# Kernel optimization log

Measured on AMD Instinct MI355X. Metric: run time of the kernel, lower is better.

Reference implementation:

```python
import jax, jax.numpy as jnp
from jax import lax
import numpy as np

B = 32768
H = 7
W = 7
EMB = 64
NUM_ACTIONS = 7
HIDDEN = 128
CNN_OUT = 64 * 3 * 3  # 576, from 7x7 input through the conv/pool stack


def setup_inputs() -> dict:
    key = jax.random.key(0)
    ks = jax.random.split(key, 20)
    frame = jax.random.randint(ks[0], (2, B, H, W, 3), 0, 11, dtype=jnp.int32)
    carried_col = jax.random.randint(ks[1], (2, B, 1), 0, 6, dtype=jnp.int32)
    carried_obj = jax.random.randint(ks[2], (2, B, 1), 0, 11, dtype=jnp.int32)

    def w(k, shape):
        return (jax.random.normal(k, shape, jnp.float32) * 0.05)

    return {
        "frame": frame,
        "carried_col": carried_col,
        "carried_obj": carried_obj,
        "conv1_w": w(ks[3], (16, 3, 2, 2)),  "conv1_b": jnp.zeros((16,), jnp.float32),
        "conv2_w": w(ks[4], (32, 16, 2, 2)), "conv2_b": jnp.zeros((32,), jnp.float32),
        "conv3_w": w(ks[5], (64, 32, 2, 2)), "conv3_b": jnp.zeros((64,), jnp.float32),
        "proj_w": w(ks[6], (EMB, CNN_OUT + 2)), "proj_b": jnp.zeros((EMB,), jnp.float32),
        "h1_w": w(ks[7], (HIDDEN, EMB * 2 + 4)), "h1_b": jnp.zeros((HIDDEN,), jnp.float32),
        "ln_g": jnp.ones((HIDDEN,), jnp.float32), "ln_b": jnp.zeros((HIDDEN,), jnp.float32),
        "h2_w": w(ks[8], (HIDDEN, HIDDEN)), "h2_b": jnp.zeros((HIDDEN,), jnp.float32),
        "h3_w": w(ks[9], (NUM_ACTIONS, HIDDEN)), "h3_b": jnp.zeros((NUM_ACTIONS,), jnp.float32),
    }


def _conv(x, wgt, b):
    # Conv2d(kernel=2, padding=1), NCHW
    y = lax.conv_general_dilated(x, wgt, (1, 1), [(1, 1), (1, 1)],
                                 dimension_numbers=("NCHW", "OIHW", "NCHW"))
    return y + b[None, :, None, None]


def _maxpool2(x):
    # MaxPool2d(2): window 2, stride 2, floor (VALID)
    return lax.reduce_window(x, -jnp.inf, lax.max, (1, 1, 2, 2), (1, 1, 2, 2), "VALID")


def _encode(fr, cc, co, p):
    x = fr.transpose(0, 3, 1, 2).astype(jnp.float32)  # [B,3,H,W]
    x = _maxpool2(jax.nn.relu(_conv(x, p["conv1_w"], p["conv1_b"])))  # [B,16,4,4]
    x = _maxpool2(jax.nn.relu(_conv(x, p["conv2_w"], p["conv2_b"])))  # [B,32,2,2]
    x = jax.nn.relu(_conv(x, p["conv3_w"], p["conv3_b"]))             # [B,64,3,3]
    feats = x.reshape(x.shape[0], -1)                                  # [B,576]
    carried = jnp.concatenate([cc, co], axis=-1).astype(jnp.float32)   # [B,2]
    comb = jnp.concatenate([feats, carried], axis=1)                   # [B,578]
    return jax.nn.relu(comb @ p["proj_w"].T + p["proj_b"])            # [B,64]


def _dir_pos(fr):
    # vectorized first-match of frame[...,0]==10 in row-major order
    b = fr.shape[0]
    mask = (fr[..., 0] == 10).reshape(b, -1)             # [B, H*W]
    has = jnp.any(mask, axis=-1)                         # [B]
    idx = jnp.argmax(mask, axis=-1)                      # first True (row-major)
    y = idx // W
    x = idx % W
    ch2 = fr[..., 2].reshape(b, -1)
    d_raw = jnp.take_along_axis(ch2, idx[:, None], axis=1)[:, 0] % 4
    d = jnp.where(has, d_raw, 0)                         # [B] int
    pos = jnp.stack([y.astype(jnp.float32) / (H - 1),
                     x.astype(jnp.float32) / (W - 1)], axis=-1)
    pos = jnp.where(has[:, None], pos, jnp.float32(0.5))  # [B,2]
    return d, pos


def _forward(frame, carried_col, carried_obj, p):
    curr_f, next_f = frame[0], frame[1]
    curr_emb = _encode(curr_f, carried_col[0], carried_obj[0], p)
    next_emb = _encode(next_f, carried_col[1], carried_obj[1], p)
    cd, cpos = _dir_pos(curr_f)
    nd, npos = _dir_pos(next_f)
    delta = ((nd - cd + 4) % 4).astype(jnp.float32)
    angle = delta * (2.0 * 3.14159 / 4.0)  # matches source constant
    dir_delta = jnp.stack([jnp.sin(angle), jnp.cos(angle)], axis=-1)  # [B,2]
    pos_delta = npos - cpos                                           # [B,2]
    comb = jnp.concatenate([curr_emb, next_emb, dir_delta, pos_delta], axis=-1)  # [B,132]
    h = comb @ p["h1_w"].T + p["h1_b"]
    mu = h.mean(-1, keepdims=True)
    var = ((h - mu) ** 2).mean(-1, keepdims=True)
    h = (h - mu) * lax.rsqrt(var + 1e-5) * p["ln_g"] + p["ln_b"]
    h = jax.nn.relu(h)  # dropout = identity in eval
    h = jax.nn.relu(h @ p["h2_w"].T + p["h2_b"])
    return h @ p["h3_w"].T + p["h3_b"]  # [B, num_actions]


def reference(frame, carried_col, carried_obj,
              conv1_w, conv1_b, conv2_w, conv2_b, conv3_w, conv3_b,
              proj_w, proj_b, h1_w, h1_b, ln_g, ln_b,
              h2_w, h2_b, h3_w, h3_b):
    p = dict(conv1_w=conv1_w, conv1_b=conv1_b, conv2_w=conv2_w, conv2_b=conv2_b,
             conv3_w=conv3_w, conv3_b=conv3_b, proj_w=proj_w, proj_b=proj_b,
             h1_w=h1_w, h1_b=h1_b, ln_g=ln_g, ln_b=ln_b,
             h2_w=h2_w, h2_b=h2_b, h3_w=h3_w, h3_b=h3_b)
    return _forward(frame, carried_col, carried_obj, p)
```

## Files before the change

### kernel.cpp

```cpp
#include <hip/hip_runtime.h>
#include <hip/hip_bf16.h>

#define BATCH 32768
#define NELEM 65536

typedef unsigned short u16;
typedef unsigned int u32;
typedef __attribute__((ext_vector_type(8))) short bf16x8;
typedef __attribute__((ext_vector_type(4))) float f32x4;

__device__ __forceinline__ float bf2f(u16 u) {
    union { u32 u; float f; } c; c.u = ((u32)u) << 16; return c.f;
}
__device__ __forceinline__ u16 f2bf(float f) {
    union { float f; u32 u; } c; c.f = f;
    u32 x = c.u;
    u32 r = (x + 0x7fffu + ((x >> 16) & 1u)) >> 16;
    return (u16)r;
}

__global__ __launch_bounds__(256) void k0_prep(const float* __restrict__ pw,
        const float* __restrict__ w2, const float* __restrict__ w3,
        const float* __restrict__ h2w, const float* __restrict__ h1w,
        const float* __restrict__ w1,
        u16* __restrict__ pwT, u16* __restrict__ w2r, u16* __restrict__ w3r,
        u16* __restrict__ h2hi, u16* __restrict__ h2lo,
        u16* __restrict__ h1hi, u16* __restrict__ h1lo,
        u16* __restrict__ w1hi, u16* __restrict__ w1lo) {
    int idx = blockIdx.x * 256 + threadIdx.x;
    if (idx < 38912) {
        int j = idx / 608, kk = idx - j * 608;
        float v = 0.f;
        if (kk < 576) {
            int p = kk >> 6, oc = kk & 63;
            v = pw[j * 578 + oc * 9 + p];
        } else if (kk < 578) {
            v = pw[j * 578 + kk];
        }
        pwT[idx] = f2bf(v);
    } else if (idx < 40960) {
        int i = idx - 38912;
        int oc = i >> 6, rem = i & 63, tap = rem >> 4, ic = rem & 15;
        w2r[i] = f2bf(w2[oc * 64 + ic * 4 + tap]);
    } else if (idx < 49152) {
        int i = idx - 40960;
        int oc = i >> 7, rem = i & 127, tap = rem >> 5, ic = rem & 31;
        w3r[i] = f2bf(w3[oc * 128 + ic * 4 + tap]);
    } else if (idx < 65536) {
        int i = idx - 49152;
        float v = h2w[i];
        u16 hi = f2bf(v);
        h2hi[i] = hi;
        h2lo[i] = f2bf(v - bf2f(hi));
    } else if (idx < 86016) {
        int i = idx - 65536;
        int j = i / 160, k = i - j * 160;
        float v = (k < 132) ? h1w[j * 132 + k] : 0.f;
        u16 hi = f2bf(v);
        h1hi[i] = hi;
        h1lo[i] = f2bf(v - bf2f(hi));
    } else if (idx < 86528) {
        int i = idx - 86016;
        int oc = i >> 5, k = i & 31;
        int ky = k >> 4, kx = (k >> 3) & 1, c = k & 7;
        float v = (c < 3) ? w1[oc * 12 + c * 4 + ky * 2 + kx] : 0.f;
        u16 hi = f2bf(v);
        w1hi[i] = hi;
        w1lo[i] = f2bf(v - bf2f(hi));
    }
}

__device__ __forceinline__ void split8(const float* __restrict__ x,
                                       bf16x8& hi, bf16x8& lo) {
    #pragma unroll
    for (int j = 0; j < 8; ++j) {
        u16 h = f2bf(x[j]);
        hi[j] = (short)h;
        lo[j] = (short)f2bf(x[j] - bf2f(h));
    }
}

__global__ __launch_bounds__(256) void kall(const int* __restrict__ frame,
        const u16* __restrict__ w1hi, const u16* __restrict__ w1lo,
        const float* __restrict__ b1,
        const u16* __restrict__ w2r, const float* __restrict__ b2,
        const u16* __restrict__ w3r, const float* __restrict__ b3,
        const int* __restrict__ ccol, const int* __restrict__ cobj,
        const u16* __restrict__ pwT, const float* __restrict__ pb,
        const u16* __restrict__ h1hi, const u16* __restrict__ h1lo,
        const float* __restrict__ h1b,
        const float* __restrict__ lng, const float* __restrict__ lnb,
        const u16* __restrict__ h2hi, const u16* __restrict__ h2lo,
        const float* __restrict__ h2b,
        const float* __restrict__ h3w, const float* __restrict__ h3b,
        float* __restrict__ out) {
    __shared__ u16 lds[24576];
    __shared__ float4 fdirL[32];
    u16* p2L   = lds;
    u16* p1L   = lds + 4096;
    u16* frL   = lds + 12288;
    u16* featL = lds + 4096;
    float* combL = (float*)lds;
    float* hL    = (float*)(lds + 4096);
    int t = threadIdx.x;
    int l = t & 63;
    int wv = t >> 6;
    int col = l & 15;
    int kg = l >> 4;
    int b0 = blockIdx.x * 16;

    #pragma unroll
    for (int i = 0; i < 6; ++i) {
        int o = i * 256 + t;
        if (o < 1312) *(uint4*)(frL + o * 8) = make_uint4(0u, 0u, 0u, 0u);
    }

    {
        bf16x8 c1hi = *(const bf16x8*)(w1hi + col * 32 + kg * 8);
        bf16x8 c1lo = *(const bf16x8*)(w1lo + col * 32 + kg * 8);
        float c1b = b1[col];
        int ky1 = kg >> 1, kx1 = kg & 1;
        bool wr1 = (kg < 2);
        for (int h = 0; h < 2; ++h) {
            __syncthreads();
            const int* fbase = frame + ((size_t)b0 + (size_t)h * BATCH) * 147;
            #pragma unroll
            for (int i = 0; i < 10; ++i) {
                int idx = i * 256 + t;
                if (idx < 2352) {
                    int le = idx / 147, r = idx - le * 147;
                    int cell = r / 3, c = r - cell * 3;
                    int y = cell / 7, x = cell - y * 7;
                    frL[le * 656 + (y + 1) * 72 + (x + 1) * 8 + c] = f2bf((float)fbase[idx]);
                }
            }
            __syncthreads();
            #pragma unroll
            for (int q = 0; q < 4; ++q) {
                int le = wv * 4 + q;
                const u16* eb = frL + le * 656;
                u16* op = p1L + (h * 16 + le) * 256;
                #pragma unroll
                for (int mt = 0; mt < 4; ++mt) {
                    int posA = mt * 16 + col;
                    int oy = posA >> 3, ox = posA & 7;
                    bf16x8 a = *(const bf16x8*)(eb + (oy + ky1) * 72 + (ox + kx1) * 8);
                    f32x4 acc = {0.f, 0.f, 0.f, 0.f};
                    acc = __builtin_amdgcn_mfma_f32_16x16x32_bf16(a, c1hi, acc, 0, 0, 0);
                    acc = __builtin_amdgcn_mfma_f32_16x16x32_bf16(a, c1lo, acc, 0, 0, 0);
                    float x0 = fmaxf(acc[0] + c1b, 0.f);
                    float x1 = fmaxf(acc[1] + c1b, 0.f);
                    float x2 = fmaxf(acc[2] + c1b, 0.f);
                    float x3 = fmaxf(acc[3] + c1b, 0.f);
                    float y0 = fmaxf(x0, x1);
                    float y1 = fmaxf(x2, x3);
                    float m0 = fmaxf(y0, __shfl_xor(y0, 32, 64));
                    float m1 = fmaxf(y1, __shfl_xor(y1, 32, 64));
                    if (wr1) {
                        op[(mt * 4 + kg * 2 + 0) * 16 + col] = f2bf(m0);
                        op[(mt * 4 + kg * 2 + 1) * 16 + col] = f2bf(m1);
                    }
                }
            }
            {
                int le = wv * 4 + kg;
                const u16* eb = frL + le * 656;
                int best = 49;
                #pragma unroll
                for (int q2 = 0; q2 < 4; ++q2) {
                    int cell = col + q2 * 16;
                    if (cell < 49) {
                        int y = cell / 7, x = cell - y * 7;
                        u16 v = eb[(y + 1) * 72 + (x + 1) * 8];
                        if (v == (u16)0x4120 && cell < best) best = cell;
                    }
                }
                best = min(best, __shfl_xor(best, 1, 64));
                best = min(best, __shfl_xor(best, 2, 64));
                best = min(best, __shfl_xor(best, 4, 64));
                best = min(best, __shfl_xor(best, 8, 64));
                if (col == 0) {
                    float dd = 0.f, py = 0.5f, px = 0.5f;
                    if (best < 49) {
                        int y = best / 7, x = best - y * 7;
                        u16 c2 = eb[(y + 1) * 72 + (x + 1) * 8 + 2];
                        dd = (float)(((int)bf2f(c2)) & 3);
                        py = (float)y / 6.0f;
                        px = (float)x / 6.0f;
                    }
                    fdirL[h * 16 + le] = make_float4(dd, py, px, 0.f);
                }
            }
        }
    }
    __syncthreads();

    {
        bf16x8 bfrag[2][2];
        #pragma unroll
        for (int s = 0; s < 2; ++s)
            #pragma unroll
            for (int nt = 0; nt < 2; ++nt)
                bfrag[s][nt] = *(const bf16x8*)(w2r + (nt * 16 + col) * 64 + s * 32 + kg * 8);
        float bias2[2] = { b2[col], b2[16 + col] };
        int oy = col >> 2, ox = col & 3;
        int aoff[2]; bool aok[2];
        #pragma unroll
        for (int s = 0; s < 2; ++s) {
            int tap = 2 * s + (kg >> 1);
            int ky = tap >> 1, kx = tap & 1;
            int iy = oy - 1 + ky, ix = ox - 1 + kx;
            aok[s] = (iy >= 0 && ix >= 0);
            aoff[s] = (iy * 4 + ix) * 16 + (kg & 1) * 8;
        }
        #pragma unroll
        for (int q = 0; q < 8; ++q) {
            int e = wv * 8 + q;
            const u16* pbase = p1L + e * 256;
            bf16x8 a0 = {0,0,0,0,0,0,0,0}, a1 = {0,0,0,0,0,0,0,0};
            if (aok[0]) a0 = *(const bf16x8*)(pbase + aoff[0]);
            if (aok[1]) a1 = *(const bf16x8*)(pbase + aoff[1]);
            f32x4 acc0 = {0.f,0.f,0.f,0.f}, acc1 = {0.f,0.f,0.f,0.f};
            acc0 = __builtin_amdgcn_mfma_f32_16x16x32_bf16(a0, bfrag[0][0], acc0, 0, 0, 0);
            acc1 = __builtin_amdgcn_mfma_f32_16x16x32_bf16(a0, bfrag[0][1], acc1, 0, 0, 0);
            acc0 = __builtin_amdgcn_mfma_f32_16x16x32_bf16(a1, bfrag[1][0], acc0, 0, 0, 0);
            acc1 = __builtin_amdgcn_mfma_f32_16x16x32_bf16(a1, bfrag[1][1], acc1, 0, 0, 0);
            #pragma unroll
            for (int nt = 0; nt < 2; ++nt) {
                f32x4 acc = nt ? acc1 : acc0;
                float b = bias2[nt];
                float m0 = fmaxf(fmaxf(acc[0] + b, 0.f), fmaxf(acc[1] + b, 0.f));
                float m1 = fmaxf(fmaxf(acc[2] + b, 0.f), fmaxf(acc[3] + b, 0.f));
                float p0 = fmaxf(m0, __shfl_xor(m0, 16, 64));
                float p1 = fmaxf(m1, __shfl_xor(m1, 16, 64));
                if ((kg & 1) == 0) {
                    int qq = (kg >> 1) * 2;
                    u16* op = p2L + e * 128 + nt * 16 + col;
                    op[qq * 32]       = f2bf(p0);
                    op[(qq + 1) * 32] = f2bf(p1);
                }
            }
        }
    }
    __syncthreads();

    int colhi = col >> 3, collo = col & 7;
    {
        bf16x8 bfrag[4][4];
        #pragma unroll
        for (int s = 0; s < 4; ++s)
            #pragma unroll
            for (int nt = 0; nt < 4; ++nt)
                bfrag[s][nt] = *(const bf16x8*)(w3r + (nt * 16 + col) * 128 + s * 32 + kg * 8);
        float bias[4];
        #pragma unroll
        for (int nt = 0; nt < 4; ++nt) bias[nt] = b3[nt * 16 + col];

        auto do_tile = [&](int i) {
            int m0 = i * 16;
            int m = m0 + col;
            u32 elem = (u32)(((unsigned long long)(u32)m * 954437177ull) >> 33);
            int p = m - (int)elem * 9;
            int oy = (p * 86) >> 8;
            int ox = p - 3 * oy;
            const u16* pbase = p2L + elem * 128 + kg * 8;
            f32x4 acc[4];
            #pragma unroll
            for (int nt = 0; nt < 4; ++nt) {
                acc[nt][0] = 0.f; acc[nt][1] = 0.f; acc[nt][2] = 0.f; acc[nt][3] = 0.f;
            }
            #pragma unroll
            for (int s = 0; s < 4; ++s) {
                int ky = s >> 1, kx = s & 1;
                int iy = oy - 1 + ky, ix = ox - 1 + kx;
                bf16x8 a = {0,0,0,0,0,0,0,0};
                if (iy >= 0 && iy <= 1 && ix >= 0 && ix <= 1)
                    a = *(const bf16x8*)(pbase + (iy * 2 + ix) * 32);
                #pragma unroll
                for (int nt = 0; nt < 4; ++nt)
                    acc[nt] = __builtin_amdgcn_mfma_f32_16x16x32_bf16(a, bfrag[s][nt], acc[nt], 0, 0, 0);
            }
            #pragma unroll
            for (int r = 0; r < 4; ++r) {
                int mr = m0 + kg * 4 + r;
                u32 er = (u32)(((unsigned long long)(u32)mr * 954437177ull) >> 33);
                int pr = mr - (int)er * 9;
                int e7 = (int)(er & 7u);
                u16* fb = featL + er * 640 + collo;
                #pragma unroll
                for (int nt = 0; nt < 4; ++nt) {
                    int blk = (pr * 8 + nt * 2 + colhi) ^ e7;
                    fb[blk * 8] = f2bf(fmaxf(acc[nt][r] + bias[nt], 0.f));
                }
            }
        };
        #pragma unroll
        for (int u = 0; u < 4; ++u) do_tile(wv + u * 4);
        if (wv < 2) do_tile(16 + wv);
    }
    if (t < 32) {
        int g = b0 + (t >> 4) * BATCH + (t & 15);
        union { u16 s[8]; uint4 q; } b;
        b.s[0] = f2bf((float)ccol[g]);
        b.s[1] = f2bf((float)cobj[g]);
        #pragma unroll
        for (int i = 2; i < 8; ++i) b.s[i] = 0;
        *(uint4*)(featL + t * 640 + (72 ^ (t & 7)) * 8) = b.q;
    }
    __syncthreads();

    {
        int rh = wv & 1, nh = wv >> 1;
        const u16* arowb = featL + (rh * 16 + col) * 640;
        int rx = col & 7;
        const u16* brow = pwT + (nh * 32 + col) * 608 + kg * 8;
        f32x4 acc0 = {0.f,0.f,0.f,0.f}, acc1 = {0.f,0.f,0.f,0.f};
        #pragma unroll
        for (int k0 = 0; k0 < 608; k0 += 32) {
            bf16x8 a;
            if (k0 + kg * 8 < 584) {
                int L = (k0 >> 3) + kg;
                a = *(const bf16x8*)(arowb + (L ^ rx) * 8);
            } else {
                #pragma unroll
                for (int j = 0; j < 8; ++j) a[j] = 0;
            }
            bf16x8 b0f = *(const bf16x8*)(brow + k0);
            bf16x8 b1f = *(const bf16x8*)(brow + 16 * 608 + k0);
            acc0 = __builtin_amdgcn_mfma_f32_16x16x32_bf16(a, b0f, acc0, 0, 0, 0);
            acc1 = __builtin_amdgcn_mfma_f32_16x16x32_bf16(a, b1f, acc1, 0, 0, 0);
        }
        __syncthreads();
        #pragma unroll
        for (int nt = 0; nt < 2; ++nt) {
            int n = nh * 32 + nt * 16 + col;
            float pbv = pb[n];
            f32x4 acc = nt ? acc1 : acc0;
            #pragma unroll
            for (int r = 0; r < 4; ++r) {
                combL[(kg * 4 + r) * 128 + rh * 64 + n] = fmaxf(acc[r] + pbv, 0.f);
            }
        }
    }
    __syncthreads();

    {
        const float* arow = combL + col * 128 + kg * 8;
        f32x4 acc[2];
        acc[0][0]=0.f; acc[0][1]=0.f; acc[0][2]=0.f; acc[0][3]=0.f;
        acc[1][0]=0.f; acc[1][1]=0.f; acc[1][2]=0.f; acc[1][3]=0.f;
        #pragma unroll
        for (int s = 0; s < 5; ++s) {
            float x[8];
            if (s < 4) {
                #pragma unroll
                for (int j = 0; j < 8; ++j) x[j] = arow[s * 32 + j];
            } else {
                #pragma unroll
                for (int j = 0; j < 8; ++j) x[j] = 0.f;
                if (kg == 0) {
                    float4 f0 = fdirL[col];
                    float4 f1 = fdirL[16 + col];
                    int delta = (((int)f1.x) - ((int)f0.x) + 4) & 3;
                    const float ANG = (float)(2.0 * 3.14159 / 4.0);
                    float angle = (float)delta * ANG;
                    x[0] = sinf(angle);
                    x[1] = cosf(angle);
                    x[2] = f1.y - f0.y;
                    x[3] = f1.z - f0.z;
                }
            }
            bf16x8 ahi, alo;
            split8(x, ahi, alo);
            #pragma unroll
            for (int nt = 0; nt < 2; ++nt) {
                int n0 = (wv * 2 + nt) * 16 + col;
                bf16x8 bhiF = *(const bf16x8*)(h1hi + n0 * 160 + s * 32 + kg * 8);
                bf16x8 bloF = *(const bf16x8*)(h1lo + n0 * 160 + s * 32 + kg * 8);
                acc[nt] = __builtin_amdgcn_mfma_f32_16x16x32_bf16(ahi, bhiF, acc[nt], 0, 0, 0);
                acc[nt] = __builtin_amdgcn_mfma_f32_16x16x32_bf16(alo, bhiF, acc[nt], 0, 0, 0);
                acc[nt] = __builtin_amdgcn_mfma_f32_16x16x32_bf16(ahi, bloF, acc[nt], 0, 0, 0);
            }
        }
        #pragma unroll
        for (int nt = 0; nt < 2; ++nt) {
            int n = (wv * 2 + nt) * 16 + col;
            float bv = h1b[n];
            #pragma unroll
            for (int r = 0; r < 4; ++r)
                hL[(kg * 4 + r) * 132 + n] = acc[nt][r] + bv;
        }
    }
    __syncthreads();

    #pragma unroll
    for (int rr = 0; rr < 4; ++rr) {
        float* rp = hL + (wv * 4 + rr) * 132 + l * 2;
        float2 v = *(const float2*)rp;
        float s = v.x + v.y;
        s += __shfl_xor(s, 1, 64);
        s += __shfl_xor(s, 2, 64);
        s += __shfl_xor(s, 4, 64);
        s += __shfl_xor(s, 8, 64);
        s += __shfl_xor(s, 16, 64);
        s += __shfl_xor(s, 32, 64);
        float mu = s * (1.0f / 128.0f);
        float d0 = v.x - mu, d1 = v.y - mu;
        float vs = d0 * d0 + d1 * d1;
        vs += __shfl_xor(vs, 1, 64);
        vs += __shfl_xor(vs, 2, 64);
        vs += __shfl_xor(vs, 4, 64);
        vs += __shfl_xor(vs, 8, 64);
        vs += __shfl_xor(vs, 16, 64);
        vs += __shfl_xor(vs, 32, 64);
        float rs = rsqrtf(vs * (1.0f / 128.0f) + 1e-5f);
        float2 o;
        o.x = fmaxf(d0 * rs * lng[l * 2]     + lnb[l * 2],     0.f);
        o.y = fmaxf(d1 * rs * lng[l * 2 + 1] + lnb[l * 2 + 1], 0.f);
        *(float2*)rp = o;
    }
    __syncthreads();

    {
        const float* arow = hL + col * 132 + kg * 8;
        f32x4 acc[2];
        acc[0][0]=0.f; acc[0][1]=0.f; acc[0][2]=0.f; acc[0][3]=0.f;
        acc[1][0]=0.f; acc[1][1]=0.f; acc[1][2]=0.f; acc[1][3]=0.f;
        #pragma unroll
        for (int s = 0; s < 4; ++s) {
            float x[8];
            #pragma unroll
            for (int j = 0; j < 8; ++j) x[j] = arow[s * 32 + j];
            bf16x8 ahi, alo;
            split8(x, ahi, alo);
            #pragma unroll
            for (int nt = 0; nt < 2; ++nt) {
                int n0 = (wv * 2 + nt) * 16 + col;
                bf16x8 bhiF = *(const bf16x8*)(h2hi + n0 * 128 + s * 32 + kg * 8);
                bf16x8 bloF = *(const bf16x8*)(h2lo + n0 * 128 + s * 32 + kg * 8);
                acc[nt] = __builtin_amdgcn_mfma_f32_16x16x32_bf16(ahi, bhiF, acc[nt], 0, 0, 0);
                acc[nt] = __builtin_amdgcn_mfma_f32_16x16x32_bf16(alo, bhiF, acc[nt], 0, 0, 0);
                acc[nt] = __builtin_amdgcn_mfma_f32_16x16x32_bf16(ahi, bloF, acc[nt], 0, 0, 0);
            }
        }
        __syncthreads();
        #pragma unroll
        for (int nt = 0; nt < 2; ++nt) {
            int n = (wv * 2 + nt) * 16 + col;
            float bv = h2b[n];
            #pragma unroll
            for (int r = 0; r < 4; ++r)
                hL[(kg * 4 + r) * 132 + n] = fmaxf(acc[nt][r] + bv, 0.f);
        }
    }
    __syncthreads();

    if (t < 112) {
        int row = t / 7, j = t - row * 7;
        const float* rp = hL + row * 132;
        float a0 = h3b[j];
        const float* wr0 = h3w + j * 128;
        #pragma unroll 4
        for (int c = 0; c < 32; ++c) {
            float4 v = *(const float4*)(rp + c * 4);
            a0 += v.x * wr0[c * 4 + 0];
            a0 += v.y * wr0[c * 4 + 1];
            a0 += v.z * wr0[c * 4 + 2];
            a0 += v.w * wr0[c * 4 + 3];
        }
        out[(size_t)(b0 + row) * 7 + j] = a0;
    }
}

extern "C" void kernel_launch(void* const* d_in, const int* in_sizes, int n_in,
                              void* d_out, int out_size, void* d_ws, size_t ws_size,
                              hipStream_t stream) {
    const int*   frame = (const int*)d_in[0];
    const int*   ccol  = (const int*)d_in[1];
    const int*   cobj  = (const int*)d_in[2];
    const float* w1    = (const float*)d_in[3];
    const float* b1    = (const float*)d_in[4];
    const float* w2    = (const float*)d_in[5];
    const float* b2    = (const float*)d_in[6];
    const float* w3    = (const float*)d_in[7];
    const float* b3    = (const float*)d_in[8];
    const float* pw    = (const float*)d_in[9];
    const float* pb    = (const float*)d_in[10];
    const float* h1w   = (const float*)d_in[11];
    const float* h1b   = (const float*)d_in[12];
    const float* lng   = (const float*)d_in[13];
    const float* lnb   = (const float*)d_in[14];
    const float* h2w   = (const float*)d_in[15];
    const float* h2b   = (const float*)d_in[16];
    const float* h3w   = (const float*)d_in[17];
    const float* h3b   = (const float*)d_in[18];
    float* out = (float*)d_out;

    char* ws = (char*)d_ws;
    u16*   pwT      = (u16*)(ws + 0);
    u16*   w2r      = (u16*)(ws + 131072);
    u16*   w3r      = (u16*)(ws + 139264);
    u16*   h2hi     = (u16*)(ws + 163840);
    u16*   h2lo     = (u16*)(ws + 196608);
    u16*   h1hi     = (u16*)(ws + 229376);
    u16*   h1lo     = (u16*)(ws + 270336);
    u16*   w1hi     = (u16*)(ws + 311296);
    u16*   w1lo     = (u16*)(ws + 312320);

    k0_prep<<<340, 256, 0, stream>>>(pw, w2, w3, h2w, h1w, w1,
                                     pwT, w2r, w3r, h2hi, h2lo, h1hi, h1lo,
                                     w1hi, w1lo);
    kall<<<2048, 256, 0, stream>>>(frame, w1hi, w1lo, b1, w2r, b2,
                                   w3r, b3, ccol, cobj, pwT, pb,
                                   h1hi, h1lo, h1b, lng, lnb,
                                   h2hi, h2lo, h2b, h3w, h3b, out);
}
```

Baseline: 222.5 us.

## Double block threads, compact frame layout, pre-split bf16 activations in LDS for MLP

Raises the block size from 256 to 512 threads with launch bounds of (512, 6) and shrinks LDS use. The frame layout is compacted to 4 channels per cell, and both frames are loaded in a single pass with vectorized bf16 conversion. The per-wave split of MLP work is redistributed, and the XOR swizzle on the feature buffer is removed in favor of a 584-stride layout. Activations for h1 and h2 are stored in LDS already split into hi/lo bf16, so the per-lane split8 conversion disappears. The trade-offs are possible LDS bank conflicts from the dropped swizzle and tighter register budgets at the higher occupancy target.

```diff
diff --git a/kernel.cpp b/kernel.cpp
--- a/kernel.cpp
+++ b/kernel.cpp
@@ -2,7 +2,6 @@
 #include <hip/hip_bf16.h>
 
 #define BATCH 32768
-#define NELEM 65536
 
 typedef unsigned short u16;
 typedef unsigned int u32;
@@ -17,6 +16,10 @@
     u32 x = c.u;
     u32 r = (x + 0x7fffu + ((x >> 16) & 1u)) >> 16;
     return (u16)r;
+}
+__device__ __forceinline__ u16 i2bf(int v) {
+    union { float f; u32 u; } c; c.f = (float)v;
+    return (u16)(c.u >> 16);
 }
 
 __global__ __launch_bounds__(256) void k0_prep(const float* __restrict__ pw,
@@ -62,25 +65,15 @@
     } else if (idx < 86528) {
         int i = idx - 86016;
         int oc = i >> 5, k = i & 31;
-        int ky = k >> 4, kx = (k >> 3) & 1, c = k & 7;
-        float v = (c < 3) ? w1[oc * 12 + c * 4 + ky * 2 + kx] : 0.f;
+        int ky = k >> 3, kx = (k >> 2) & 1, c = k & 3;
+        float v = (ky < 2 && c < 3) ? w1[oc * 12 + c * 4 + ky * 2 + kx] : 0.f;
         u16 hi = f2bf(v);
         w1hi[i] = hi;
         w1lo[i] = f2bf(v - bf2f(hi));
     }
 }
 
-__device__ __forceinline__ void split8(const float* __restrict__ x,
-                                       bf16x8& hi, bf16x8& lo) {
-    #pragma unroll
-    for (int j = 0; j < 8; ++j) {
-        u16 h = f2bf(x[j]);
-        hi[j] = (short)h;
-        lo[j] = (short)f2bf(x[j] - bf2f(h));
-    }
-}
-
-__global__ __launch_bounds__(256) void kall(const int* __restrict__ frame,
+__global__ __launch_bounds__(512, 6) void kall(const int* __restrict__ frame,
         const u16* __restrict__ w1hi, const u16* __restrict__ w1lo,
         const float* __restrict__ b1,
         const u16* __restrict__ w2r, const float* __restrict__ b2,
@@ -94,102 +87,120 @@
         const float* __restrict__ h2b,
         const float* __restrict__ h3w, const float* __restrict__ h3b,
         float* __restrict__ out) {
-    __shared__ u16 lds[24576];
+    __shared__ u16 lds[22784];
     __shared__ float4 fdirL[32];
-    u16* p2L   = lds;
-    u16* p1L   = lds + 4096;
-    u16* frL   = lds + 12288;
-    u16* featL = lds + 4096;
-    float* combL = (float*)lds;
-    float* hL    = (float*)(lds + 4096);
+    u16* p2L    = lds;
+    u16* p1L    = lds + 4096;
+    u16* frL4   = lds + 12288;
+    u16* featL  = lds + 4096;
+    u16* combHi = lds;
+    u16* combLo = lds + 2560;
+    float* hL   = (float*)(lds + 5120);
+    u16* hLhi   = lds + 9344;
+    u16* hLlo   = lds + 11904;
+
     int t = threadIdx.x;
     int l = t & 63;
     int wv = t >> 6;
     int col = l & 15;
     int kg = l >> 4;
+    int wq = wv & 3, wh = wv >> 2;
     int b0 = blockIdx.x * 16;
 
     #pragma unroll
-    for (int i = 0; i < 6; ++i) {
-        int o = i * 256 + t;
-        if (o < 1312) *(uint4*)(frL + o * 8) = make_uint4(0u, 0u, 0u, 0u);
-    }
+    for (int i = 0; i < 3; ++i) {
+        int o = i * 512 + t;
+        if (o < 1312) *(uint4*)(frL4 + o * 8) = make_uint4(0u, 0u, 0u, 0u);
+    }
+    __syncthreads();
+
+    #pragma unroll
+    for (int i = 0; i < 4; ++i) {
+        int c = i * 512 + t;
+        if (c < 1568) {
+            int le = c / 49, rem = c - le * 49;
+            int y = rem / 7, x = rem - y * 7;
+            const int* fp = frame
+                + ((size_t)b0 + (size_t)(le & 15) + (size_t)(le >> 4) * BATCH) * 147
+                + rem * 3;
+            int v0 = fp[0], v1 = fp[1], v2 = fp[2];
+            uint2 st;
+            st.x = (u32)i2bf(v0) | ((u32)i2bf(v1) << 16);
+            st.y = (u32)i2bf(v2);
+            *(uint2*)(frL4 + le * 328 + (y + 1) * 36 + (x + 1) * 4) = st;
+        }
+    }
+    __syncthreads();
 
     {
         bf16x8 c1hi = *(const bf16x8*)(w1hi + col * 32 + kg * 8);
         bf16x8 c1lo = *(const bf16x8*)(w1lo + col * 32 + kg * 8);
         float c1b = b1[col];
-        int ky1 = kg >> 1, kx1 = kg & 1;
         bool wr1 = (kg < 2);
-        for (int h = 0; h < 2; ++h) {
-            __syncthreads();
-            const int* fbase = frame + ((size_t)b0 + (size_t)h * BATCH) * 147;
-            #pragma unroll
-            for (int i = 0; i < 10; ++i) {
-                int idx = i * 256 + t;
-                if (idx < 2352) {
-                    int le = idx / 147, r = idx - le * 147;
-                    int cell = r / 3, c = r - cell * 3;
+        #pragma unroll
+        for (int q = 0; q < 4; ++q) {
+            int le = wh * 16 + wq * 4 + q;
+            const u16* eb = frL4 + le * 328;
+            u16* op = p1L + le * 256;
+            #pragma unroll
+            for (int mt = 0; mt < 4; ++mt) {
+                int posA = mt * 16 + col;
+                int oy = posA >> 3, ox = posA & 7;
+                bf16x8 a;
+                if (kg < 2) {
+                    const u16* ap = eb + (oy + kg) * 36 + ox * 4;
+                    union { uint2 d[2]; bf16x8 v; } uu;
+                    uu.d[0] = *(const uint2*)ap;
+                    uu.d[1] = *(const uint2*)(ap + 4);
+                    a = uu.v;
+                } else {
+                    #pragma unroll
+                    for (int j = 0; j < 8; ++j) a[j] = 0;
+                }
+                f32x4 acc = {0.f, 0.f, 0.f, 0.f};
+                acc = __builtin_amdgcn_mfma_f32_16x16x32_bf16(a, c1hi, acc, 0, 0, 0);
+                acc = __builtin_amdgcn_mfma_f32_16x16x32_bf16(a, c1lo, acc, 0, 0, 0);
+                float x0 = fmaxf(acc[0] + c1b, 0.f);
+                float x1 = fmaxf(acc[1] + c1b, 0.f);
+                float x2 = fmaxf(acc[2] + c1b, 0.f);
+                float x3 = fmaxf(acc[3] + c1b, 0.f);
+                float y0 = fmaxf(x0, x1);
+                float y1 = fmaxf(x2, x3);
+                float m0 = fmaxf(y0, __shfl_xor(y0, 32, 64));
+                float m1 = fmaxf(y1, __shfl_xor(y1, 32, 64));
+                if (wr1) {
+                    op[(mt * 4 + kg * 2 + 0) * 16 + col] = f2bf(m0);
+                    op[(mt * 4 + kg * 2 + 1) * 16 + col] = f2bf(m1);
+                }
+            }
+        }
+        {
+            int e = wh * 16 + wq * 4 + kg;
+            const u16* eb = frL4 + e * 328;
+            int best = 49;
+            #pragma unroll
+            for (int q2 = 0; q2 < 4; ++q2) {
+                int cell = col + q2 * 16;
+                if (cell < 49) {
                     int y = cell / 7, x = cell - y * 7;
-                    frL[le * 656 + (y + 1) * 72 + (x + 1) * 8 + c] = f2bf((float)fbase[idx]);
+                    u16 v = eb[(y + 1) * 36 + (x + 1) * 4];
+                    if (v == (u16)0x4120 && cell < best) best = cell;
                 }
             }
-            __syncthreads();
-            #pragma unroll
-            for (int q = 0; q < 4; ++q) {
-                int le = wv * 4 + q;
-                const u16* eb = frL + le * 656;
-                u16* op = p1L + (h * 16 + le) * 256;
-                #pragma unroll
-                for (int mt = 0; mt < 4; ++mt) {
-                    int posA = mt * 16 + col;
-                    int oy = posA >> 3, ox = posA & 7;
-                    bf16x8 a = *(const bf16x8*)(eb + (oy + ky1) * 72 + (ox + kx1) * 8);
-                    f32x4 acc = {0.f, 0.f, 0.f, 0.f};
-                    acc = __builtin_amdgcn_mfma_f32_16x16x32_bf16(a, c1hi, acc, 0, 0, 0);
-                    acc = __builtin_amdgcn_mfma_f32_16x16x32_bf16(a, c1lo, acc, 0, 0, 0);
-                    float x0 = fmaxf(acc[0] + c1b, 0.f);
-                    float x1 = fmaxf(acc[1] + c1b, 0.f);
-                    float x2 = fmaxf(acc[2] + c1b, 0.f);
-                    float x3 = fmaxf(acc[3] + c1b, 0.f);
-                    float y0 = fmaxf(x0, x1);
-                    float y1 = fmaxf(x2, x3);
-                    float m0 = fmaxf(y0, __shfl_xor(y0, 32, 64));
-                    float m1 = fmaxf(y1, __shfl_xor(y1, 32, 64));
-                    if (wr1) {
-                        op[(mt * 4 + kg * 2 + 0) * 16 + col] = f2bf(m0);
-                        op[(mt * 4 + kg * 2 + 1) * 16 + col] = f2bf(m1);
-                    }
+            best = min(best, __shfl_xor(best, 1, 64));
+            best = min(best, __shfl_xor(best, 2, 64));
+            best = min(best, __shfl_xor(best, 4, 64));
+            best = min(best, __shfl_xor(best, 8, 64));
+            if (col == 0) {
+                float dd = 0.f, py = 0.5f, px = 0.5f;
+                if (best < 49) {
+                    int y = best / 7, x = best - y * 7;
+                    u16 c2 = eb[(y + 1) * 36 + (x + 1) * 4 + 2];
+                    dd = (float)(((int)bf2f(c2)) & 3);
+                    py = (float)y / 6.0f;
+                    px = (float)x / 6.0f;
                 }
-            }
-            {
-                int le = wv * 4 + kg;
-                const u16* eb = frL + le * 656;
-                int best = 49;
-                #pragma unroll
-                for (int q2 = 0; q2 < 4; ++q2) {
-                    int cell = col + q2 * 16;
-                    if (cell < 49) {
-                        int y = cell / 7, x = cell - y * 7;
-                        u16 v = eb[(y + 1) * 72 + (x + 1) * 8];
-                        if (v == (u16)0x4120 && cell < best) best = cell;
-                    }
-                }
-                best = min(best, __shfl_xor(best, 1, 64));
-                best = min(best, __shfl_xor(best, 2, 64));
-                best = min(best, __shfl_xor(best, 4, 64));
-                best = min(best, __shfl_xor(best, 8, 64));
-                if (col == 0) {
-                    float dd = 0.f, py = 0.5f, px = 0.5f;
-                    if (best < 49) {
-                        int y = best / 7, x = best - y * 7;
-                        u16 c2 = eb[(y + 1) * 72 + (x + 1) * 8 + 2];
-                        dd = (float)(((int)bf2f(c2)) & 3);
-                        py = (float)y / 6.0f;
-                        px = (float)x / 6.0f;
-                    }
-                    fdirL[h * 16 + le] = make_float4(dd, py, px, 0.f);
-                }
+                fdirL[e] = make_float4(dd, py, px, 0.f);
             }
         }
     }
@@ -214,8 +225,8 @@
             aoff[s] = (iy * 4 + ix) * 16 + (kg & 1) * 8;
         }
         #pragma unroll
-        for (int q = 0; q < 8; ++q) {
-            int e = wv * 8 + q;
+        for (int q = 0; q < 4; ++q) {
+            int e = wv * 4 + q;
             const u16* pbase = p1L + e * 256;
             bf16x8 a0 = {0,0,0,0,0,0,0,0}, a1 = {0,0,0,0,0,0,0,0};
             if (aok[0]) a0 = *(const bf16x8*)(pbase + aoff[0]);
@@ -285,17 +296,16 @@
                 int mr = m0 + kg * 4 + r;
                 u32 er = (u32)(((unsigned long long)(u32)mr * 954437177ull) >> 33);
                 int pr = mr - (int)er * 9;
-                int e7 = (int)(er & 7u);
-                u16* fb = featL + er * 640 + collo;
+                u16* fb = featL + er * 584 + collo;
                 #pragma unroll
                 for (int nt = 0; nt < 4; ++nt) {
-                    int blk = (pr * 8 + nt * 2 + colhi) ^ e7;
+                    int blk = pr * 8 + nt * 2 + colhi;
                     fb[blk * 8] = f2bf(fmaxf(acc[nt][r] + bias[nt], 0.f));
                 }
             }
         };
-        #pragma unroll
-        for (int u = 0; u < 4; ++u) do_tile(wv + u * 4);
+        do_tile(wv);
+        do_tile(8 + wv);
         if (wv < 2) do_tile(16 + wv);
     }
     if (t < 32) {
@@ -305,97 +315,88 @@
         b.s[1] = f2bf((float)cobj[g]);
         #pragma unroll
         for (int i = 2; i < 8; ++i) b.s[i] = 0;
-        *(uint4*)(featL + t * 640 + (72 ^ (t & 7)) * 8) = b.q;
+        *(uint4*)(featL + t * 584 + 576) = b.q;
     }
     __syncthreads();
 
     {
-        int rh = wv & 1, nh = wv >> 1;
-        const u16* arowb = featL + (rh * 16 + col) * 640;
-        int rx = col & 7;
-        const u16* brow = pwT + (nh * 32 + col) * 608 + kg * 8;
-        f32x4 acc0 = {0.f,0.f,0.f,0.f}, acc1 = {0.f,0.f,0.f,0.f};
+        int rh = wv & 1, nf = wv >> 1;
+        const u16* arowb = featL + (rh * 16 + col) * 584;
+        const u16* brow  = pwT + (nf * 16 + col) * 608 + kg * 8;
+        f32x4 accA = {0.f,0.f,0.f,0.f}, accB = {0.f,0.f,0.f,0.f};
         #pragma unroll
         for (int k0 = 0; k0 < 608; k0 += 32) {
             bf16x8 a;
             if (k0 + kg * 8 < 584) {
-                int L = (k0 >> 3) + kg;
-                a = *(const bf16x8*)(arowb + (L ^ rx) * 8);
+                a = *(const bf16x8*)(arowb + k0 + kg * 8);
             } else {
                 #pragma unroll
                 for (int j = 0; j < 8; ++j) a[j] = 0;
             }
-            bf16x8 b0f = *(const bf16x8*)(brow + k0);
-            bf16x8 b1f = *(const bf16x8*)(brow + 16 * 608 + k0);
-            acc0 = __builtin_amdgcn_mfma_f32_16x16x32_bf16(a, b0f, acc0, 0, 0, 0);
-            acc1 = __builtin_amdgcn_mfma_f32_16x16x32_bf16(a, b1f, acc1, 0, 0, 0);
+            bf16x8 b = *(const bf16x8*)(brow + k0);
+            if ((k0 >> 5) & 1)
+                accB = __builtin_amdgcn_mfma_f32_16x16x32_bf16(a, b, accB, 0, 0, 0);
+            else
+                accA = __builtin_amdgcn_mfma_f32_16x16x32_bf16(a, b, accA, 0, 0, 0);
         }
         __syncthreads();
-        #pragma unroll
-        for (int nt = 0; nt < 2; ++nt) {
-            int n = nh * 32 + nt * 16 + col;
+        if (t < 16) {
+            float4 f0 = fdirL[t];
+            float4 f1 = fdirL[16 + t];
+            int delta = (((int)f1.x) - ((int)f0.x) + 4) & 3;
+            const float ANG = (float)(2.0 * 3.14159 / 4.0);
+            float ang = (float)delta * ANG;
+            float xs[4] = { sinf(ang), cosf(ang), f1.y - f0.y, f1.z - f0.z };
+            #pragma unroll
+            for (int j = 0; j < 4; ++j) {
+                u16 hi = f2bf(xs[j]);
+                combHi[t * 160 + 128 + j] = hi;
+                combLo[t * 160 + 128 + j] = f2bf(xs[j] - bf2f(hi));
+            }
+        }
+        {
+            int n = nf * 16 + col;
             float pbv = pb[n];
-            f32x4 acc = nt ? acc1 : acc0;
             #pragma unroll
             for (int r = 0; r < 4; ++r) {
-                combL[(kg * 4 + r) * 128 + rh * 64 + n] = fmaxf(acc[r] + pbv, 0.f);
+                float v = fmaxf(accA[r] + accB[r] + pbv, 0.f);
+                u16 hi = f2bf(v);
+                int off = (kg * 4 + r) * 160 + rh * 64 + n;
+                combHi[off] = hi;
+                combLo[off] = f2bf(v - bf2f(hi));
             }
         }
     }
     __syncthreads();
 
     {
-        const float* arow = combL + col * 128 + kg * 8;
-        f32x4 acc[2];
-        acc[0][0]=0.f; acc[0][1]=0.f; acc[0][2]=0.f; acc[0][3]=0.f;
-        acc[1][0]=0.f; acc[1][1]=0.f; acc[1][2]=0.f; acc[1][3]=0.f;
+        const u16* ah = combHi + col * 160 + kg * 8;
+        const u16* al = combLo + col * 160 + kg * 8;
+        int n = wv * 16 + col;
+        const u16* bh = h1hi + n * 160 + kg * 8;
+        const u16* bl = h1lo + n * 160 + kg * 8;
+        f32x4 accP = {0.f,0.f,0.f,0.f}, accQ = {0.f,0.f,0.f,0.f};
         #pragma unroll
         for (int s = 0; s < 5; ++s) {
-            float x[8];
-            if (s < 4) {
-                #pragma unroll
-                for (int j = 0; j < 8; ++j) x[j] = arow[s * 32 + j];
-            } else {
-                #pragma unroll
-                for (int j = 0; j < 8; ++j) x[j] = 0.f;
-                if (kg == 0) {
-                    float4 f0 = fdirL[col];
-                    float4 f1 = fdirL[16 + col];
-                    int delta = (((int)f1.x) - ((int)f0.x) + 4) & 3;
-                    const float ANG = (float)(2.0 * 3.14159 / 4.0);
-                    float angle = (float)delta * ANG;
-                    x[0] = sinf(angle);
-                    x[1] = cosf(angle);
-                    x[2] = f1.y - f0.y;
-                    x[3] = f1.z - f0.z;
-                }
-            }
-            bf16x8 ahi, alo;
-            split8(x, ahi, alo);
-            #pragma unroll
-            for (int nt = 0; nt < 2; ++nt) {
-                int n0 = (wv * 2 + nt) * 16 + col;
-                bf16x8 bhiF = *(const bf16x8*)(h1hi + n0 * 160 + s * 32 + kg * 8);
-                bf16x8 bloF = *(const bf16x8*)(h1lo + n0 * 160 + s * 32 + kg * 8);
-                acc[nt] = __builtin_amdgcn_mfma_f32_16x16x32_bf16(ahi, bhiF, acc[nt], 0, 0, 0);
-                acc[nt] = __builtin_amdgcn_mfma_f32_16x16x32_bf16(alo, bhiF, acc[nt], 0, 0, 0);
-                acc[nt] = __builtin_amdgcn_mfma_f32_16x16x32_bf16(ahi, bloF, acc[nt], 0, 0, 0);
-            }
-        }
-        #pragma unroll
-        for (int nt = 0; nt < 2; ++nt) {
-            int n = (wv * 2 + nt) * 16 + col;
-            float bv = h1b[n];
-            #pragma unroll
-            for (int r = 0; r < 4; ++r)
-                hL[(kg * 4 + r) * 132 + n] = acc[nt][r] + bv;
-        }
+            bf16x8 Ah = *(const bf16x8*)(ah + s * 32);
+            bf16x8 Al = *(const bf16x8*)(al + s * 32);
+            bf16x8 Bh = *(const bf16x8*)(bh + s * 32);
+            bf16x8 Bl = *(const bf16x8*)(bl + s * 32);
+            accP = __builtin_amdgcn_mfma_f32_16x16x32_bf16(Ah, Bh, accP, 0, 0, 0);
+            accQ = __builtin_amdgcn_mfma_f32_16x16x32_bf16(Al, Bh, accQ, 0, 0, 0);
+            accQ = __builtin_amdgcn_mfma_f32_16x16x32_bf16(Ah, Bl, accQ, 0, 0, 0);
+        }
+        float bv = h1b[n];
+        #pragma unroll
+        for (int r = 0; r < 4; ++r)
+            hL[(kg * 4 + r) * 132 + n] = accP[r] + accQ[r] + bv;
     }
     __syncthreads();
 
     #pragma unroll
-    for (int rr = 0; rr < 4; ++rr) {
-        float* rp = hL + (wv * 4 + rr) * 132 + l * 2;
+    for (int rr = 0; rr < 2; ++rr) {
+        int row = wv * 2 + rr;
+        float* rp = hL + row * 132 + l * 2;
         float2 v = *(const float2*)rp;
         float s = v.x + v.y;
         s += __shfl_xor(s, 1, 64);
@@ -414,59 +415,49 @@
         vs += __shfl_xor(vs, 16, 64);
         vs += __shfl_xor(vs, 32, 64);
         float rs = rsqrtf(vs * (1.0f / 128.0f) + 1e-5f);
-        float2 o;
-        o.x = fmaxf(d0 * rs * lng[l * 2]     + lnb[l * 2],     0.f);
-        o.y = fmaxf(d1 * rs * lng[l * 2 + 1] + lnb[l * 2 + 1], 0.f);
-        *(float2*)rp = o;
+        float o0 = fmaxf(d0 * rs * lng[l * 2]     + lnb[l * 2],     0.f);
+        float o1 = fmaxf(d1 * rs * lng[l * 2 + 1] + lnb[l * 2 + 1], 0.f);
+        u16 h0 = f2bf(o0), h1v = f2bf(o1);
+        *(u32*)(hLhi + row * 160 + l * 2) = (u32)h0 | ((u32)h1v << 16);
+        u16 l0 = f2bf(o0 - bf2f(h0)), l1v = f2bf(o1 - bf2f(h1v));
+        *(u32*)(hLlo + row * 160 + l * 2) = (u32)l0 | ((u32)l1v << 16);
     }
     __syncthreads();
 
     {
-        const float* arow = hL + col * 132 + kg * 8;
-        f32x4 acc[2];
-        acc[0][0]=0.f; acc[0][1]=0.f; acc[0][2]=0.f; acc[0][3]=0.f;
-        acc[1][0]=0.f; acc[1][1]=0.f; acc[1][2]=0.f; acc[1][3]=0.f;
+        const u16* ah = hLhi + col * 160 + kg * 8;
+        const u16* al = hLlo + col * 160 + kg * 8;
+        int n = wv * 16 + col;
+        const u16* bh = h2hi + n * 128 + kg * 8;
+        const u16* bl = h2lo + n * 128 + kg * 8;
+        f32x4 accP = {0.f,0.f,0.f,0.f}, accQ = {0.f,0.f,0.f,0.f};
         #pragma unroll
         for (int s = 0; s < 4; ++s) {
-            float x[8];
-            #pragma unroll
-            for (int j = 0; j < 8; ++j) x[j] = arow[s * 32 + j];
-            bf16x8 ahi, alo;
-            split8(x, ahi, alo);
-            #pragma unroll
-            for (int nt = 0; nt < 2; ++nt) {
-                int n0 = (wv * 2 + nt) * 16 + col;
-                bf16x8 bhiF = *(const bf16x8*)(h2hi + n0 * 128 + s * 32 + kg * 8);
-                bf16x8 bloF = *(const bf16x8*)(h2lo + n0 * 128 + s * 32 + kg * 8);
-                acc[nt] = __builtin_amdgcn_mfma_f32_16x16x32_bf16(ahi, bhiF, acc[nt], 0, 0, 0);
-                acc[nt] = __builtin_amdgcn_mfma_f32_16x16x32_bf16(alo, bhiF, acc[nt], 0, 0, 0);
-                acc[nt] = __builtin_amdgcn_mfma_f32_16x16x32_bf16(ahi, bloF, acc[nt], 0, 0, 0);
-            }
-        }
-        __syncthreads();
-        #pragma unroll
-        for (int nt = 0; nt < 2; ++nt) {
-            int n = (wv * 2 + nt) * 16 + col;
-            float bv = h2b[n];
-            #pragma unroll
-            for (int r = 0; r < 4; ++r)
-                hL[(kg * 4 + r) * 132 + n] = fmaxf(acc[nt][r] + bv, 0.f);
-        }
+            bf16x8 Ah = *(const bf16x8*)(ah + s * 32);
+            bf16x8 Al = *(const bf16x8*)(al + s * 32);
+            bf16x8 Bh = *(const bf16x8*)(bh + s * 32);
+            bf16x8 Bl = *(const bf16x8*)(bl + s * 32);
+            accP = __builtin_amdgcn_mfma_f32_16x16x32_bf16(Ah, Bh, accP, 0, 0, 0);
+            accQ = __builtin_amdgcn_mfma_f32_16x16x32_bf16(Al, Bh, accQ, 0, 0, 0);
+            accQ = __builtin_amdgcn_mfma_f32_16x16x32_bf16(Ah, Bl, accQ, 0, 0, 0);
+        }
+        float bv = h2b[n];
+        #pragma unroll
+        for (int r = 0; r < 4; ++r)
+            hL[(kg * 4 + r) * 132 + n] = fmaxf(accP[r] + accQ[r] + bv, 0.f);
     }
     __syncthreads();
 
     if (t < 112) {
         int row = t / 7, j = t - row * 7;
         const float* rp = hL + row * 132;
+        const float* wr0 = h3w + j * 128;
         float a0 = h3b[j];
-        const float* wr0 = h3w + j * 128;
         #pragma unroll 4
         for (int c = 0; c < 32; ++c) {
             float4 v = *(const float4*)(rp + c * 4);
-            a0 += v.x * wr0[c * 4 + 0];
-            a0 += v.y * wr0[c * 4 + 1];
-            a0 += v.z * wr0[c * 4 + 2];
-            a0 += v.w * wr0[c * 4 + 3];
+            float4 w = *(const float4*)(wr0 + c * 4);
+            a0 += v.x * w.x + v.y * w.y + v.z * w.z + v.w * w.w;
         }
         out[(size_t)(b0 + row) * 7 + j] = a0;
     }
@@ -510,7 +501,7 @@
     k0_prep<<<340, 256, 0, stream>>>(pw, w2, w3, h2w, h1w, w1,
                                      pwT, w2r, w3r, h2hi, h2lo, h1hi, h1lo,
                                      w1hi, w1lo);
-    kall<<<2048, 256, 0, stream>>>(frame, w1hi, w1lo, b1, w2r, b2,
+    kall<<<2048, 512, 0, stream>>>(frame, w1hi, w1lo, b1, w2r, b2,
                                    w3r, b3, ccol, cobj, pwT, pb,
                                    h1hi, h1lo, h1b, lng, lnb,
                                    h2hi, h2lo, h2b, h3w, h3b, out);
```

Result: slower. 261.2 us (+17.4%).
